# Optimization experiments

Measured on AMD Instinct MI355X. Metric: run time of the kernel, lower is better.

## Reference

```python
import jax, jax.numpy as jnp
import numpy as np

NUM_HEAD = 16
EMBD_DIM = 2048
LATENT_DIM = 512
ROPE_DIM = 64  # min(rope_dim, head_dim) = 64
HEAD_DIM = EMBD_DIM // NUM_HEAD  # 128
ROPE_HALF = ROPE_DIM // 2
SCALE = (HEAD_DIM + ROPE_DIM) ** -0.5


def setup_inputs() -> dict:
    key = jax.random.key(0)
    ks = jax.random.split(key, 9)
    B, S = 2, 2048
    std = 0.02
    return {
        "x": jax.random.normal(ks[0], (B, S, EMBD_DIM), dtype=jnp.float32),
        "w_ckv": jax.random.normal(ks[1], (EMBD_DIM, LATENT_DIM), dtype=jnp.float32) * std,
        "w_k": jax.random.normal(ks[2], (LATENT_DIM, EMBD_DIM), dtype=jnp.float32) * std,
        "w_v": jax.random.normal(ks[3], (LATENT_DIM, EMBD_DIM), dtype=jnp.float32) * std,
        "w_cq": jax.random.normal(ks[4], (EMBD_DIM, LATENT_DIM), dtype=jnp.float32) * std,
        "w_q": jax.random.normal(ks[5], (LATENT_DIM, EMBD_DIM), dtype=jnp.float32) * std,
        "w_qr": jax.random.normal(ks[6], (LATENT_DIM, NUM_HEAD * ROPE_DIM), dtype=jnp.float32) * std,
        "w_kr": jax.random.normal(ks[7], (EMBD_DIM, ROPE_DIM), dtype=jnp.float32) * std,
        "w_o": jax.random.normal(ks[8], (EMBD_DIM, EMBD_DIM), dtype=jnp.float32) * std,
    }


def _apply_rope(x, S):
    # x: [B, H, S, D] with D >= ROPE_DIM; interleaved even/odd rotation
    inv_freq = 1.0 / (10000.0 ** (jnp.arange(0, ROPE_DIM, 2, dtype=jnp.float32) / ROPE_DIM))
    pos = jnp.arange(S, dtype=jnp.float32)
    freqs = pos[:, None] * inv_freq[None, :]           # [S, ROPE_HALF]
    cos = jnp.cos(freqs)[None, None]                   # [1,1,S,ROPE_HALF]
    sin = jnp.sin(freqs)[None, None]
    x_rope, x_pass = x[..., :ROPE_DIM], x[..., ROPE_DIM:]
    x_even, x_odd = x_rope[..., 0::2], x_rope[..., 1::2]
    r_even = x_even * cos - x_odd * sin
    r_odd = x_even * sin + x_odd * cos
    rotated = jnp.stack([r_even, r_odd], axis=-1).reshape(x_rope.shape)
    return jnp.concatenate([rotated, x_pass], axis=-1) if x_pass.shape[-1] > 0 else rotated


def reference(x, w_ckv, w_k, w_v, w_cq, w_q, w_qr, w_kr, w_o):
    B, S, _ = x.shape
    c_kv = x @ w_ckv                                   # [B,S,latent]
    k_c = (c_kv @ w_k).reshape(B, S, NUM_HEAD, HEAD_DIM).transpose(0, 2, 1, 3)
    v = (c_kv @ w_v).reshape(B, S, NUM_HEAD, HEAD_DIM).transpose(0, 2, 1, 3)
    c_q = x @ w_cq
    q_c = (c_q @ w_q).reshape(B, S, NUM_HEAD, HEAD_DIM).transpose(0, 2, 1, 3)
    q_r = (c_q @ w_qr).reshape(B, S, NUM_HEAD, ROPE_DIM).transpose(0, 2, 1, 3)
    k_r = (x @ w_kr)[:, None, :, :]                    # [B,1,S,rope] shared across heads
    k_r = jnp.broadcast_to(k_r, (B, NUM_HEAD, S, ROPE_DIM))
    q_r = _apply_rope(q_r, S)
    k_r = _apply_rope(k_r, S)
    q = jnp.concatenate([q_c, q_r], axis=-1)           # [B,H,S,head+rope]
    k = jnp.concatenate([k_c, k_r], axis=-1)
    scores = jnp.einsum("bhsd,bhtd->bhst", q, k) * SCALE
    causal = jnp.tril(jnp.ones((S, S), dtype=bool))
    scores = jnp.where(causal[None, None], scores, -jnp.inf)
    attn = jax.nn.softmax(scores, axis=-1)
    out = jnp.einsum("bhst,bhtd->bhsd", attn, v)       # [B,H,S,head]
    out = out.transpose(0, 2, 1, 3).reshape(B, S, EMBD_DIM)
    return out @ w_o
```

## Files before the change

kernel.cpp:

```cpp
#include <hip/hip_runtime.h>


typedef unsigned short u16;
typedef __attribute__((ext_vector_type(8))) short s16x8;
typedef __attribute__((ext_vector_type(4))) float f32x4;
typedef __attribute__((ext_vector_type(8))) __bf16 bf16x8;
typedef __attribute__((ext_vector_type(4))) u16 u16x4;

#define S_LEN 2048
#define NH 16
#define HD 128
#define DQK 192
#define EMB 2048

#define GLOAD_LDS16(g, l)                                                      \
  __builtin_amdgcn_global_load_lds(                                            \
      (const __attribute__((address_space(1))) unsigned int*)(g),              \
      (__attribute__((address_space(3))) unsigned int*)(l), 16, 0, 0)

__device__ __forceinline__ u16 f2b(float f) {
  unsigned u = __builtin_bit_cast(unsigned, f);
  u += 0x7FFFu + ((u >> 16) & 1u);
  return (u16)(u >> 16);
}
__device__ __forceinline__ float b2f(u16 v) {
  unsigned u = ((unsigned)v) << 16;
  return __builtin_bit_cast(float, u);
}
__device__ __forceinline__ bf16x8 ld_bf8(const u16* p) {
  return __builtin_bit_cast(bf16x8, *(const s16x8*)p);
}

__device__ __forceinline__ void transpose_tile(const float* __restrict__ in,
                                               u16* __restrict__ out,
                                               int K, int N, int local, int t,
                                               u16* T ) {
  int nt = N >> 6;
  int n0 = (local % nt) * 64, k0 = (local / nt) * 64;
#pragma unroll
  for (int r = 0; r < 4; ++r) {
    int kl = (t >> 4) + r * 16, nl = (t & 15) * 4;
    f32x4 v = *(const f32x4*)(in + (size_t)(k0 + kl) * N + n0 + nl);
#pragma unroll
    for (int j = 0; j < 4; ++j) T[(nl + j) * 72 + kl] = f2b(v[j]);
  }
  __syncthreads();
#pragma unroll
  for (int r = 0; r < 2; ++r) {
    int chunk = t + r * 256, nr = chunk >> 3, kc = (chunk & 7) * 8;
    *(s16x8*)(out + (size_t)(n0 + nr) * K + k0 + kc) = *(const s16x8*)(&T[nr * 72 + kc]);
  }
}

__global__ __launch_bounds__(256) void prep_kernel(
    const float* __restrict__ xf, u16* __restrict__ XB,
    const float* __restrict__ wckvf, u16* __restrict__ WCKV_T,
    const float* __restrict__ wcqf,  u16* __restrict__ WCQ_T,
    const float* __restrict__ wkrf,  u16* __restrict__ WKR_T,
    const float* __restrict__ wkf,   u16* __restrict__ WK_T,
    const float* __restrict__ wvf,   u16* __restrict__ WV_T,
    const float* __restrict__ wqf,   u16* __restrict__ WQ_T,
    const float* __restrict__ wqrf,  u16* __restrict__ WQR_T,
    const float* __restrict__ wof,   u16* __restrict__ WO_T,
    float* __restrict__ cosT, float* __restrict__ sinT) {
  __shared__ u16 T[64 * 72];
  const int id = blockIdx.x, t = threadIdx.x;
  if (id < 8192) {
    int i = id * 256 + t;
    f32x4 v = *(const f32x4*)(xf + (size_t)i * 4);
    u16x4 o = { f2b(v[0]), f2b(v[1]), f2b(v[2]), f2b(v[3]) };
    *(u16x4*)(XB + (size_t)i * 4) = o;
  } else if (id < 8448)  { transpose_tile(wckvf, WCKV_T, 2048, 512,  id - 8192, t, T); }
  else if (id < 8704)    { transpose_tile(wcqf,  WCQ_T,  2048, 512,  id - 8448, t, T); }
  else if (id < 8736)    { transpose_tile(wkrf,  WKR_T,  2048, 64,   id - 8704, t, T); }
  else if (id < 8992)    { transpose_tile(wkf,   WK_T,   512,  2048, id - 8736, t, T); }
  else if (id < 9248)    { transpose_tile(wvf,   WV_T,   512,  2048, id - 8992, t, T); }
  else if (id < 9504)    { transpose_tile(wqf,   WQ_T,   512,  2048, id - 9248, t, T); }
  else if (id < 9632)    { transpose_tile(wqrf,  WQR_T,  512,  1024, id - 9504, t, T); }
  else if (id < 10656)   { transpose_tile(wof,   WO_T,   2048, 2048, id - 9632, t, T); }
  else {
    int i2 = (id - 10656) * 256 + t;
    int s = i2 >> 5, i = i2 & 31;
    float inv = exp2f(-(float)i * (13.287712379549449f / 32.0f));
    float ang = (float)s * inv;
    cosT[i2] = cosf(ang);
    sinT[i2] = sinf(ang);
  }
}

template<int MODE>
__global__ __launch_bounds__(256) void gemm_bt_kernel(const u16* __restrict__ A,
                                                      int lda,
                                                      const u16* __restrict__ BT,
                                                      void* __restrict__ Cout,
                                                      void* __restrict__ Cout2,
                                                      int M, int N, int K,
                                                      float scale) {
  __shared__ __align__(16) u16 As[2][128 * 64];
  __shared__ __align__(16) u16 Bs[2][128 * 64];
  const int t = threadIdx.x;
  const int lane = t & 63, wid = t >> 6;
  const int wr = (wid >> 1) * 64, wc = (wid & 1) * 64;
  const int bm0 = blockIdx.y * 128, bn0 = blockIdx.x * 128;
  const int lr = lane & 15, lg = lane >> 4;

  auto stage = [&](int k0, int buf) {
#pragma unroll
    for (int r = 0; r < 4; ++r) {
      int chunk = t + r * 256;
      int row = chunk >> 3, kcs = (chunk & 7) * 8;
      int kcg = kcs ^ ((row & 7) << 3);
      GLOAD_LDS16(A + (size_t)(bm0 + row) * lda + k0 + kcg, &As[buf][chunk * 8]);
      GLOAD_LDS16(BT + (size_t)(bn0 + row) * K + k0 + kcg, &Bs[buf][chunk * 8]);
    }
  };

  f32x4 acc[4][4] = {};
  const int nt = K >> 6;
  stage(0, 0);
  for (int tk = 0; tk < nt; ++tk) {
    const int cur = tk & 1;
    __syncthreads();
    if (tk + 1 < nt) stage((tk + 1) << 6, cur ^ 1);
#pragma unroll
    for (int kk = 0; kk < 2; ++kk) {
      bf16x8 af[4], bfr[4];
      const int kbase = kk * 32 + lg * 8;
#pragma unroll
      for (int m = 0; m < 4; ++m) {
        int row = wr + m * 16 + lr;
        af[m] = ld_bf8(&As[cur][row * 64 + (kbase ^ ((row & 7) << 3))]);
      }
#pragma unroll
      for (int n = 0; n < 4; ++n) {
        int row = wc + n * 16 + lr;
        bfr[n] = ld_bf8(&Bs[cur][row * 64 + (kbase ^ ((row & 7) << 3))]);
      }
#pragma unroll
      for (int m = 0; m < 4; ++m)
#pragma unroll
        for (int n = 0; n < 4; ++n)
          acc[m][n] = __builtin_amdgcn_mfma_f32_16x16x32_bf16(af[m], bfr[n], acc[m][n], 0, 0, 0);
    }
  }

#pragma unroll
  for (int m = 0; m < 4; ++m)
#pragma unroll
    for (int n = 0; n < 4; ++n)
#pragma unroll
      for (int rg = 0; rg < 4; ++rg) {
        int row = bm0 + wr + m * 16 + lg * 4 + rg;
        int col = bn0 + wc + n * 16 + lr;
        if (col >= N) continue;
        float v = acc[m][n][rg];
        if (MODE == 0) {
          ((u16*)Cout)[(size_t)row * N + col] = f2b(v * scale);
        } else if (MODE == 1) {
          ((float*)Cout)[(size_t)row * N + col] = v * scale;
        } else if (MODE == 4) {
          int bb = row >> 11, s = row & 2047;
          if (col < 2048) {
            int h = col >> 7, d = col & 127;
            ((u16*)Cout)[((size_t)(bb * NH + h) * S_LEN + s) * DQK + d] = f2b(v);
          } else {
            int c2 = col - 2048, h = c2 >> 7, d = c2 & 127;
            ((u16*)Cout2)[((size_t)(bb * NH + h) * HD + d) * S_LEN + s] = f2b(v);
          }
        } else {
          int bb = row >> 11, s = row & 2047;
          if (col < 2048) {
            int h = col >> 7, d = col & 127;
            ((u16*)Cout)[((size_t)(bb * NH + h) * S_LEN + s) * DQK + d] = f2b(v * scale);
          } else {
            ((u16*)Cout2)[(size_t)row * 1024 + (col - 2048)] = f2b(v);
          }
        }
      }
}

__global__ __launch_bounds__(256) void rope_assemble_kernel(const u16* __restrict__ qr,
                                                            const u16* __restrict__ cc,
                                                            const float* __restrict__ cosT,
                                                            const float* __restrict__ sinT,
                                                            u16* __restrict__ Qcat,
                                                            u16* __restrict__ Kcat) {
  int id = blockIdx.x * 256 + threadIdx.x;
  int i = id & 31;
  int s = (id >> 5) & 2047;
  int h = (id >> 16) & 15;
  int b = id >> 20;
  float c = cosT[(s << 5) + i], sn = sinT[(s << 5) + i];
  const float SC = 0.07216878364870323f;

  size_t qbase = ((size_t)b * S_LEN + s) * 1024 + h * 64 + 2 * i;
  float qe = b2f(qr[qbase]), qo = b2f(qr[qbase + 1]);
  size_t obase = ((size_t)(b * NH + h) * S_LEN + s) * DQK + HD + 2 * i;
  Qcat[obase]     = f2b((qe * c - qo * sn) * SC);
  Qcat[obase + 1] = f2b((qe * sn + qo * c) * SC);

  size_t kbase = ((size_t)b * S_LEN + s) * 1088 + 1024 + 2 * i;
  float ke = b2f(cc[kbase]), ko = b2f(cc[kbase + 1]);
  Kcat[obase]     = f2b(ke * c - ko * sn);
  Kcat[obase + 1] = f2b(ke * sn + ko * c);
}

__global__ __launch_bounds__(512, 2) void attn_kernel(const u16* __restrict__ Q,
                                                      const u16* __restrict__ K,
                                                      const u16* __restrict__ VT,
                                                      u16* __restrict__ O) {
  __shared__ u16 Ks[64 * 200];
  __shared__ u16 Vs[128 * 72];
  __shared__ u16 Ps[8 * 16 * 88];
  const int id = blockIdx.x;
  const int p8 = id >> 5, hb = id & 31;
  const int h = hb & 15, b = hb >> 4;
  const int qb = (p8 < 8) ? p8 : 23 - p8;
  const int q0 = qb * 128;
  const int t = threadIdx.x, lane = t & 63, wid = t >> 6;
  const int lr = lane & 15, lg = lane >> 4;
  const size_t qk_head = (size_t)(b * NH + h) * S_LEN * DQK;
  const size_t vt_head = (size_t)(b * NH + h) * HD * S_LEN;

  s16x8 kst[3], vst[2];
  auto gload = [&](int kt) {
#pragma unroll
    for (int r = 0; r < 3; ++r) {
      int chunk = t + r * 512, row = chunk / 24, cc = chunk % 24;
      kst[r] = *(const s16x8*)(K + qk_head + (size_t)(kt * 64 + row) * DQK + cc * 8);
    }
#pragma unroll
    for (int r = 0; r < 2; ++r) {
      int chunk = t + r * 512, d = chunk >> 3, cc = chunk & 7;
      vst[r] = *(const s16x8*)(VT + vt_head + (size_t)d * S_LEN + kt * 64 + cc * 8);
    }
  };
  auto swr = [&]() {
#pragma unroll
    for (int r = 0; r < 3; ++r) {
      int chunk = t + r * 512, row = chunk / 24, cc = chunk % 24;
      *(s16x8*)(&Ks[row * 200 + cc * 8]) = kst[r];
    }
#pragma unroll
    for (int r = 0; r < 2; ++r) {
      int chunk = t + r * 512, d = chunk >> 3, cc = chunk & 7;
      *(s16x8*)(&Vs[d * 72 + cc * 8]) = vst[r];
    }
  };

  bf16x8 qa[6];
  {
    const u16* qrow = Q + qk_head + (size_t)(q0 + wid * 16 + lr) * DQK;
#pragma unroll
    for (int ks = 0; ks < 6; ++ks) qa[ks] = ld_bf8(qrow + ks * 32 + lg * 8);
  }

  f32x4 acc_o[8] = {};
  float m_r[4] = { -INFINITY, -INFINITY, -INFINITY, -INFINITY };
  float l_r[4] = { 0.f, 0.f, 0.f, 0.f };

  const int nt = 2 * qb + 2;
  gload(0);
#pragma unroll 1
  for (int kt = 0; kt < nt; ++kt) {
    __syncthreads();
    swr();
    if (kt + 1 < nt) gload(kt + 1);
    __syncthreads();

    f32x4 sacc[4];
#pragma unroll
    for (int cb = 0; cb < 4; ++cb) {
      f32x4 sv = {};
#pragma unroll
      for (int ks = 0; ks < 6; ++ks) {
        bf16x8 kb = ld_bf8(&Ks[(cb * 16 + lr) * 200 + ks * 32 + lg * 8]);
        sv = __builtin_amdgcn_mfma_f32_16x16x32_bf16(qa[ks], kb, sv, 0, 0, 0);
      }
      sacc[cb] = sv;
    }

    if (kt >= 2 * qb) {
#pragma unroll
      for (int cb = 0; cb < 4; ++cb)
#pragma unroll
        for (int rg = 0; rg < 4; ++rg) {
          int q_g = q0 + wid * 16 + lg * 4 + rg;
          int kv_g = kt * 64 + cb * 16 + lr;
          if (kv_g > q_g) sacc[cb][rg] = -INFINITY;
        }
    }

    float pmax[4];
#pragma unroll
    for (int rg = 0; rg < 4; ++rg)
      pmax[rg] = fmaxf(fmaxf(sacc[0][rg], sacc[1][rg]), fmaxf(sacc[2][rg], sacc[3][rg]));
#pragma unroll
    for (int off = 1; off < 16; off <<= 1)
#pragma unroll
      for (int rg = 0; rg < 4; ++rg)
        pmax[rg] = fmaxf(pmax[rg], __shfl_xor(pmax[rg], off, 64));

    float alpha[4];
#pragma unroll
    for (int rg = 0; rg < 4; ++rg) {
      float mn = fmaxf(m_r[rg], pmax[rg]);
      alpha[rg] = __expf(m_r[rg] - mn);
      m_r[rg] = mn;
      l_r[rg] *= alpha[rg];
    }
#pragma unroll
    for (int vb = 0; vb < 8; ++vb)
#pragma unroll
      for (int rg = 0; rg < 4; ++rg)
        acc_o[vb][rg] *= alpha[rg];

    float psum[4] = { 0.f, 0.f, 0.f, 0.f };
#pragma unroll
    for (int cb = 0; cb < 4; ++cb)
#pragma unroll
      for (int rg = 0; rg < 4; ++rg) {
        float pv = __expf(sacc[cb][rg] - m_r[rg]);
        sacc[cb][rg] = pv;
        psum[rg] += pv;
      }
#pragma unroll
    for (int off = 1; off < 16; off <<= 1)
#pragma unroll
      for (int rg = 0; rg < 4; ++rg)
        psum[rg] += __shfl_xor(psum[rg], off, 64);
#pragma unroll
    for (int rg = 0; rg < 4; ++rg) l_r[rg] += psum[rg];

    u16* psw = &Ps[wid * (16 * 88)];
#pragma unroll
    for (int cb = 0; cb < 4; ++cb)
#pragma unroll
      for (int rg = 0; rg < 4; ++rg)
        psw[(lg * 4 + rg) * 88 + cb * 16 + lr] = f2b(sacc[cb][rg]);

    bf16x8 pa[2];
#pragma unroll
    for (int ks = 0; ks < 2; ++ks) pa[ks] = ld_bf8(&psw[lr * 88 + ks * 32 + lg * 8]);
#pragma unroll
    for (int vb = 0; vb < 8; ++vb) {
#pragma unroll
      for (int ks = 0; ks < 2; ++ks) {
        bf16x8 vv = ld_bf8(&Vs[(vb * 16 + lr) * 72 + ks * 32 + lg * 8]);
        acc_o[vb] = __builtin_amdgcn_mfma_f32_16x16x32_bf16(pa[ks], vv, acc_o[vb], 0, 0, 0);
      }
    }
  }

#pragma unroll
  for (int vb = 0; vb < 8; ++vb)
#pragma unroll
    for (int rg = 0; rg < 4; ++rg) {
      int s_glob = q0 + wid * 16 + lg * 4 + rg;
      int col = vb * 16 + lr;
      O[((size_t)b * S_LEN + s_glob) * EMB + h * HD + col] = f2b(acc_o[vb][rg] / l_r[rg]);
    }
}

extern "C" void kernel_launch(void* const* d_in, const int* in_sizes, int n_in,
                              void* d_out, int out_size, void* d_ws, size_t ws_size,
                              hipStream_t stream) {
  const float* xf    = (const float*)d_in[0];
  const float* wckvf = (const float*)d_in[1];
  const float* wkf   = (const float*)d_in[2];
  const float* wvf   = (const float*)d_in[3];
  const float* wcqf  = (const float*)d_in[4];
  const float* wqf   = (const float*)d_in[5];
  const float* wqrf  = (const float*)d_in[6];
  const float* wkrf  = (const float*)d_in[7];
  const float* wof   = (const float*)d_in[8];
  (void)in_sizes; (void)n_in; (void)out_size; (void)ws_size;

  u16* ws = (u16*)d_ws;
  size_t off = 0;
  auto alloc = [&](size_t n) -> u16* { u16* p = ws + off; off += n; return p; };
  u16* XB     = alloc(8388608);
  u16* WCKV_T = alloc(1048576);
  u16* WCQ_T  = alloc(1048576);
  u16* WKR_T  = alloc(131072);
  u16* WK_T   = alloc(1048576);
  u16* WV_T   = alloc(1048576);
  u16* WQ_T   = alloc(1048576);
  u16* WQR_T  = alloc(524288);
  u16* WO_T   = alloc(4194304);
  u16* CC     = alloc(4456448);
  u16* QR     = alloc(4194304);
  u16* QCAT   = alloc(12582912);
  u16* KCAT   = alloc(12582912);
  u16* VT     = alloc(8388608);
  u16* AOUT   = alloc(8388608);
  float* COS_T = (float*)alloc(131072);
  float* SIN_T = (float*)alloc(131072);

  prep_kernel<<<10912, 256, 0, stream>>>(xf, XB,
                                         wckvf, WCKV_T, wcqf, WCQ_T, wkrf, WKR_T,
                                         wkf, WK_T, wvf, WV_T, wqf, WQ_T,
                                         wqrf, WQR_T, wof, WO_T,
                                         COS_T, SIN_T);

  const float SC = 0.07216878364870323f;
  gemm_bt_kernel<0><<<dim3(9, 32),  256, 0, stream>>>(XB, 2048, WCKV_T, CC, nullptr,
                                                      4096, 1088, 2048, 1.0f);
  gemm_bt_kernel<4><<<dim3(32, 32), 256, 0, stream>>>(CC, 1088, WK_T, KCAT, VT,
                                                      4096, 4096, 512, 1.0f);
  gemm_bt_kernel<5><<<dim3(24, 32), 256, 0, stream>>>(CC + 512, 1088, WQ_T, QCAT, QR,
                                                      4096, 3072, 512, SC);

  rope_assemble_kernel<<<8192, 256, 0, stream>>>(QR, CC, COS_T, SIN_T, QCAT, KCAT);

  attn_kernel<<<512, 512, 0, stream>>>(QCAT, KCAT, VT, AOUT);

  gemm_bt_kernel<1><<<dim3(16, 32), 256, 0, stream>>>(AOUT, 2048, WO_T, d_out, nullptr,
                                                      4096, 2048, 2048, 1.0f);
}
```

Baseline: 271.6 us.

## Merge KV and Q up-projection GEMMs, add XCD-aware block remap, lazy softmax rescale

Combines the K/V and Q up-projection GEMMs into a single launch that dispatches on output column range, offsetting the A pointer for the Q half. Converts GEMM grids to 1-D with an XCD-interleaved block remapping to improve L2 locality. In attention, skips the running-max rescale of the accumulator unless some row's max grows by more than a threshold, trading slight numerical headroom for fewer multiplies and exps.

```diff
diff --git a/kernel.cpp b/kernel.cpp
--- a/kernel.cpp
+++ b/kernel.cpp
@@ -92,16 +92,23 @@
 __global__ __launch_bounds__(256) void gemm_bt_kernel(const u16* __restrict__ A,
                                                       int lda,
                                                       const u16* __restrict__ BT,
-                                                      void* __restrict__ Cout,
-                                                      void* __restrict__ Cout2,
+                                                      void* __restrict__ C0,
+                                                      void* __restrict__ C1,
+                                                      void* __restrict__ C2,
+                                                      void* __restrict__ C3,
                                                       int M, int N, int K,
-                                                      float scale) {
+                                                      int nx, float scale) {
   __shared__ __align__(16) u16 As[2][128 * 64];
   __shared__ __align__(16) u16 Bs[2][128 * 64];
   const int t = threadIdx.x;
   const int lane = t & 63, wid = t >> 6;
   const int wr = (wid >> 1) * 64, wc = (wid & 1) * 64;
-  const int bm0 = blockIdx.y * 128, bn0 = blockIdx.x * 128;
+  const int cpx = gridDim.x >> 3;
+  int wg = blockIdx.x;
+  wg = (wg & 7) * cpx + (wg >> 3);
+  const int bn0 = (wg % nx) * 128;
+  const int bm0 = (wg / nx) * 128;
+  if (MODE == 6 && bn0 >= 4096) A += 512;
   const int lr = lane & 15, lg = lane >> 4;
 
   auto stage = [&](int k0, int buf) {
@@ -155,25 +162,22 @@
         if (col >= N) continue;
         float v = acc[m][n][rg];
         if (MODE == 0) {
-          ((u16*)Cout)[(size_t)row * N + col] = f2b(v * scale);
+          ((u16*)C0)[(size_t)row * N + col] = f2b(v * scale);
         } else if (MODE == 1) {
-          ((float*)Cout)[(size_t)row * N + col] = v * scale;
-        } else if (MODE == 4) {
-          int bb = row >> 11, s = row & 2047;
-          if (col < 2048) {
-            int h = col >> 7, d = col & 127;
-            ((u16*)Cout)[((size_t)(bb * NH + h) * S_LEN + s) * DQK + d] = f2b(v);
-          } else {
-            int c2 = col - 2048, h = c2 >> 7, d = c2 & 127;
-            ((u16*)Cout2)[((size_t)(bb * NH + h) * HD + d) * S_LEN + s] = f2b(v);
-          }
+          ((float*)C0)[(size_t)row * N + col] = v * scale;
         } else {
           int bb = row >> 11, s = row & 2047;
           if (col < 2048) {
             int h = col >> 7, d = col & 127;
-            ((u16*)Cout)[((size_t)(bb * NH + h) * S_LEN + s) * DQK + d] = f2b(v * scale);
+            ((u16*)C0)[((size_t)(bb * NH + h) * S_LEN + s) * DQK + d] = f2b(v);
+          } else if (col < 4096) {
+            int c2 = col - 2048, h = c2 >> 7, d = c2 & 127;
+            ((u16*)C1)[((size_t)(bb * NH + h) * HD + d) * S_LEN + s] = f2b(v);
+          } else if (col < 6144) {
+            int c3 = col - 4096, h = c3 >> 7, d = c3 & 127;
+            ((u16*)C2)[((size_t)(bb * NH + h) * S_LEN + s) * DQK + d] = f2b(v * scale);
           } else {
-            ((u16*)Cout2)[(size_t)row * 1024 + (col - 2048)] = f2b(v);
+            ((u16*)C3)[(size_t)row * 1024 + (col - 6144)] = f2b(v);
           }
         }
       }
@@ -301,19 +305,23 @@
       for (int rg = 0; rg < 4; ++rg)
         pmax[rg] = fmaxf(pmax[rg], __shfl_xor(pmax[rg], off, 64));
 
-    float alpha[4];
-#pragma unroll
-    for (int rg = 0; rg < 4; ++rg) {
-      float mn = fmaxf(m_r[rg], pmax[rg]);
-      alpha[rg] = __expf(m_r[rg] - mn);
-      m_r[rg] = mn;
-      l_r[rg] *= alpha[rg];
-    }
-#pragma unroll
-    for (int vb = 0; vb < 8; ++vb)
-#pragma unroll
-      for (int rg = 0; rg < 4; ++rg)
-        acc_o[vb][rg] *= alpha[rg];
+    int nochange = (pmax[0] <= m_r[0] + 8.f) & (pmax[1] <= m_r[1] + 8.f) &
+                   (pmax[2] <= m_r[2] + 8.f) & (pmax[3] <= m_r[3] + 8.f);
+    if (!__all(nochange)) {
+      float alpha[4];
+#pragma unroll
+      for (int rg = 0; rg < 4; ++rg) {
+        float mn = fmaxf(m_r[rg], pmax[rg]);
+        alpha[rg] = __expf(m_r[rg] - mn);
+        m_r[rg] = mn;
+        l_r[rg] *= alpha[rg];
+      }
+#pragma unroll
+      for (int vb = 0; vb < 8; ++vb)
+#pragma unroll
+        for (int rg = 0; rg < 4; ++rg)
+          acc_o[vb][rg] *= alpha[rg];
+    }
 
     float psum[4] = { 0.f, 0.f, 0.f, 0.f };
 #pragma unroll
@@ -404,17 +412,17 @@
                                          COS_T, SIN_T);
 
   const float SC = 0.07216878364870323f;
-  gemm_bt_kernel<0><<<dim3(9, 32),  256, 0, stream>>>(XB, 2048, WCKV_T, CC, nullptr,
-                                                      4096, 1088, 2048, 1.0f);
-  gemm_bt_kernel<4><<<dim3(32, 32), 256, 0, stream>>>(CC, 1088, WK_T, KCAT, VT,
-                                                      4096, 4096, 512, 1.0f);
-  gemm_bt_kernel<5><<<dim3(24, 32), 256, 0, stream>>>(CC + 512, 1088, WQ_T, QCAT, QR,
-                                                      4096, 3072, 512, SC);
+  gemm_bt_kernel<0><<<288, 256, 0, stream>>>(XB, 2048, WCKV_T, CC,
+                                             nullptr, nullptr, nullptr,
+                                             4096, 1088, 2048, 9, 1.0f);
+  gemm_bt_kernel<6><<<1792, 256, 0, stream>>>(CC, 1088, WK_T, KCAT, VT, QCAT, QR,
+                                              4096, 7168, 512, 56, SC);
 
   rope_assemble_kernel<<<8192, 256, 0, stream>>>(QR, CC, COS_T, SIN_T, QCAT, KCAT);
 
   attn_kernel<<<512, 512, 0, stream>>>(QCAT, KCAT, VT, AOUT);
 
-  gemm_bt_kernel<1><<<dim3(16, 32), 256, 0, stream>>>(AOUT, 2048, WO_T, d_out, nullptr,
-                                                      4096, 2048, 2048, 1.0f);
-}
+  gemm_bt_kernel<1><<<512, 256, 0, stream>>>(AOUT, 2048, WO_T, d_out,
+                                             nullptr, nullptr, nullptr,
+                                             4096, 2048, 2048, 16, 1.0f);
+}
```

New measurement: 271.0 us. No clear change (-0.2%).
